# Performance work log

Measured on AMD Instinct MI355X. Metric: run time of the kernel, lower is better.

Reference implementation:

```python
import jax, jax.numpy as jnp
import numpy as np

B, T, C, H = 128, 256, 512, 2048
STEP_SIZE = 0.001
TOTAL = 1.0 / (T - 1)                       # uniform linspace(0,1,T) interval length
STEPS_HINT = max(1, int(TOTAL / STEP_SIZE))
N_SUB = max(1, int(max(STEPS_HINT, TOTAL / STEP_SIZE)))  # = 3 fixed RK4 substeps per interval
DT = TOTAL / N_SUB


def setup_inputs() -> dict:
    key = jax.random.key(0)
    ks = jax.random.split(key, 7)
    def lin_w(k, fi, fo):
        return (jax.random.uniform(k, (fi, fo), jnp.float32, -1.0, 1.0) / np.sqrt(fi)).astype(jnp.float32)
    def lin_b(k, fi, fo):
        return (jax.random.uniform(k, (fo,), jnp.float32, -1.0, 1.0) / np.sqrt(fi)).astype(jnp.float32)
    x = jax.random.normal(ks[0], (B, T, C), jnp.float32)
    return {
        "x": x,
        "W1": lin_w(ks[1], C, H), "b1": lin_b(ks[2], C, H),
        "W2": lin_w(ks[3], H, H), "b2": lin_b(ks[4], H, H),
        "W3": lin_w(ks[5], H, C), "b3": lin_b(ks[6], H, C),
    }


def _mlp(y, W1, b1, W2, b2, W3, b3):
    # f(y) = Linear(Tanh(Linear(Tanh(Linear(y)))))
    h = jnp.tanh(y @ W1 + b1)
    h = jnp.tanh(h @ W2 + b2)
    return h @ W3 + b3


def _rk4_step(y, dt, p):
    k1 = _mlp(y, *p)
    k2 = _mlp(y + 0.5 * dt * k1, *p)
    k3 = _mlp(y + 0.5 * dt * k2, *p)
    k4 = _mlp(y + dt * k3, *p)
    return y + (dt / 6.0) * (k1 + 2.0 * k2 + 2.0 * k3 + k4)


def reference(x, W1, b1, W2, b2, W3, b3):
    p = (W1, b1, W2, b2, W3, b3)
    def interval(y, _):
        for _ in range(N_SUB):  # static, small unroll (3)
            y = _rk4_step(y, DT, p)
        return y, y
    y0 = x[:, 0, :]                                   # [B, C]
    _, ys = jax.lax.scan(interval, y0, None, length=T - 1)  # ys: [T-1, B, C]
    return jnp.concatenate([x[:, :1, :], jnp.moveaxis(ys, 0, 1)], axis=1)  # [B, T, C]
```

## Files before the change

kernel.cpp:

```cpp
#include <hip/hip_runtime.h>
#include <hip/hip_bf16.h>
#include <cstdint>

#define B_ 128
#define T_ 256
#define C_ 512
#define H_ 2048
#define NWG 256
#define NTHR 256
#define NGROUP 8
#define GSIZE 32
#define M_ 16
#define FSTRIDE 16
#define RSU1 132
#define RSS1 528
#define DT_F 0.0013071895424836601f

typedef __bf16 bf16x8 __attribute__((ext_vector_type(8)));
typedef short s16x8 __attribute__((ext_vector_type(8)));
typedef float f32x4 __attribute__((ext_vector_type(4)));
typedef unsigned long long ull;

enum : size_t {
  OFF_FLAGS = 0,
  OFF_W1P = 32768,
  OFF_W2P = OFF_W1P + (size_t)C_ * H_ * 2,
  OFF_W3P = OFF_W2P + (size_t)H_ * H_ * 2,
  OFF_U   = OFF_W3P + (size_t)H_ * C_ * 2,
  OFF_H1  = OFF_U   + (size_t)NGROUP * M_ * C_ * 2,
  OFF_H2  = OFF_H1  + (size_t)NGROUP * M_ * H_ * 2,
  WS_END  = OFF_H2  + (size_t)NGROUP * M_ * H_ * 2
};

__device__ __forceinline__ bf16x8 ld_frag(const unsigned short* p) {
  s16x8 v = *reinterpret_cast<const s16x8*>(p);
  return __builtin_bit_cast(bf16x8, v);
}
__device__ __forceinline__ bf16x8 lds_frag(const unsigned short* p) {
  s16x8 v = *reinterpret_cast<const s16x8*>(p);
  return __builtin_bit_cast(bf16x8, v);
}
__device__ __forceinline__ void st_coh16(unsigned short* p, unsigned short v) {
  __hip_atomic_store(p, v, __ATOMIC_RELAXED, __HIP_MEMORY_SCOPE_AGENT);
}
__device__ __forceinline__ f32x4 mfma16(bf16x8 a, bf16x8 b, f32x4 c) {
  return __builtin_amdgcn_mfma_f32_16x16x32_bf16(a, b, c, 0, 0, 0);
}
__device__ __forceinline__ unsigned short tobf(float f) {
  return __builtin_bit_cast(unsigned short, (__bf16)f);
}
__device__ __forceinline__ float fast_tanh(float v) {
  float e = __expf(2.0f * v);
  return 1.0f - 2.0f / (e + 1.0f);
}

__global__ void init_flags_k(unsigned* f) {
  int i = blockIdx.x * 256 + threadIdx.x;
  if (i < NGROUP * GSIZE * FSTRIDE) f[i] = 0u;
}

__global__ void swizzle_w_k(const float* __restrict__ W, unsigned short* __restrict__ Wp,
                            int N, int kblog) {
  int idx = blockIdx.x * 256 + threadIdx.x;
  int j = idx & 7;
  int l = (idx >> 3) & 63;
  int rem = idx >> 9;
  int kb = rem & ((1 << kblog) - 1);
  int nt = rem >> kblog;
  int k = kb * 32 + ((l >> 4) << 3) + j;
  int n = (nt << 4) + (l & 15);
  Wp[idx] = tobf(W[(size_t)k * N + n]);
}

__device__ __forceinline__ void bar_arrive(unsigned* gf, int gn, unsigned gen) {
  asm volatile("s_waitcnt vmcnt(0)" ::: "memory");
  __syncthreads();
  if (threadIdx.x == 0)
    __hip_atomic_store(&gf[gn * FSTRIDE], gen, __ATOMIC_RELAXED, __HIP_MEMORY_SCOPE_AGENT);
}
__device__ __forceinline__ void bar_wait(unsigned* gf, unsigned gen) {
  if (threadIdx.x < GSIZE) {
    while (__hip_atomic_load(&gf[threadIdx.x * FSTRIDE], __ATOMIC_RELAXED,
                             __HIP_MEMORY_SCOPE_AGENT) < gen)
      __builtin_amdgcn_s_sleep(1);
  }
  __syncthreads();
}

__device__ __forceinline__ void issue_u(const ull* __restrict__ g, int tid, ull v[8]) {
  #pragma unroll
  for (int j = 0; j < 8; ++j)
    v[j] = __hip_atomic_load(g + j * NTHR + tid, __ATOMIC_RELAXED, __HIP_MEMORY_SCOPE_AGENT);
}
__device__ __forceinline__ void issue_c(const ull* __restrict__ g, int tid, ull v[8]) {
  #pragma unroll
  for (int j = 0; j < 8; ++j) {
    int i = j * NTHR + tid;
    v[j] = __hip_atomic_load(g + (size_t)(i >> 7) * 512 + (i & 127),
                             __ATOMIC_RELAXED, __HIP_MEMORY_SCOPE_AGENT);
  }
}
__device__ __forceinline__ void commit(ull* __restrict__ lds, int tid, const ull v[8]) {
  #pragma unroll
  for (int j = 0; j < 8; ++j) {
    int i = j * NTHR + tid;
    lds[(i >> 7) * RSU1 + (i & 127)] = v[j];
  }
}

#define L2CHUNK(c, buf) {                                                     \
  const unsigned short* al = (const unsigned short*)atile[buf] + llo * RSS1 + lhi * 8; \
  _Pragma("unroll")                                                           \
  for (int jj = 0; jj < 8; ++jj) {                                            \
    acc0 = mfma16(lds_frag(al + (2 * jj) * 32),     w2r[(c) * 16 + 2 * jj],     acc0); \
    acc1 = mfma16(lds_frag(al + (2 * jj + 1) * 32), w2r[(c) * 16 + 2 * jj + 1], acc1); \
  } }

#define L3CHUNK(c, buf) {                                                     \
  const unsigned short* al = (const unsigned short*)atile[buf] + llo * RSS1 + lhi * 8; \
  _Pragma("unroll")                                                           \
  for (int jj = 0; jj < 2; ++jj) {                                            \
    acc0 = mfma16(lds_frag(al + (wave * 4 + 2 * jj) * 32),     w3r[(c) * 4 + 2 * jj],     acc0); \
    acc1 = mfma16(lds_frag(al + (wave * 4 + 2 * jj + 1) * 32), w3r[(c) * 4 + 2 * jj + 1], acc1); \
  } }

__global__ __launch_bounds__(NTHR, 1) void ode_persist_k(
    const float* __restrict__ x, const float* __restrict__ b1,
    const float* __restrict__ b2, const float* __restrict__ b3,
    float* __restrict__ out, unsigned char* __restrict__ ws) {
  const int wg = blockIdx.x, tid = threadIdx.x;
  const int g = wg >> 5, gn = wg & 31;
  const int wave = tid >> 6, lane = tid & 63;
  const int lhi = lane >> 4, llo = lane & 15;

  unsigned* gflags = (unsigned*)(ws + OFF_FLAGS) + g * GSIZE * FSTRIDE;
  const unsigned short* W1p = (const unsigned short*)(ws + OFF_W1P);
  const unsigned short* W2p = (const unsigned short*)(ws + OFF_W2P);
  const unsigned short* W3p = (const unsigned short*)(ws + OFF_W3P);
  const ull* ubuf_u = (const ull*)(ws + OFF_U)  + (size_t)g * (M_ * C_ / 4);
  const ull* h1_u   = (const ull*)(ws + OFF_H1) + (size_t)g * (M_ * H_ / 4);
  const ull* h2_u   = (const ull*)(ws + OFF_H2) + (size_t)g * (M_ * H_ / 4);
  unsigned short* ubuf_s = (unsigned short*)(ws + OFF_U)  + (size_t)g * M_ * C_;
  unsigned short* h1_s   = (unsigned short*)(ws + OFF_H1) + (size_t)g * M_ * H_;
  unsigned short* h2_s   = (unsigned short*)(ws + OFF_H2) + (size_t)g * M_ * H_;

  __shared__ alignas(16) ull atile[2][M_ * RSU1];
  __shared__ float red[4][256];
  __shared__ float ytile[256], k1t[256], k2t[256], k3t[256];

  const int n16 = gn * 4 + wave;
  const unsigned short* bp1 = W1p + (size_t)n16 * 16 * 512 + lane * 8;
  const unsigned short* bp2 = W2p + (size_t)n16 * 64 * 512 + lane * 8;
  const unsigned short* bp3 = W3p + (size_t)gn  * 64 * 512 + lane * 8;

  bf16x8 w2r[64], w3r[16];
  #pragma unroll
  for (int kb = 0; kb < 64; ++kb) w2r[kb] = ld_frag(bp2 + kb * 512);
  #pragma unroll
  for (int q = 0; q < 16; ++q)
    w3r[q] = ld_frag(bp3 + ((q >> 2) * 16 + wave * 4 + (q & 3)) * 512);

  const float bb1 = b1[n16 * 16 + llo];
  const float bb2 = b2[n16 * 16 + llo];
  const float bb3 = b3[gn * 16 + llo];

  {
    int row = tid >> 4, c16 = tid & 15;
    int col = gn * 16 + c16;
    int b = g * M_ + row;
    float v = x[(size_t)b * (T_ * C_) + col];
    ytile[tid] = v;
    out[(size_t)b * (T_ * C_) + col] = v;
    st_coh16(&ubuf_s[row * C_ + col], tobf(v));
  }
  unsigned gen = 0;
  bar_arrive(gflags, gn, ++gen);
  bar_wait(gflags, gen);

  ull va[8], vb[8];
  #pragma unroll 1
  for (int t = 0; t < T_ - 1; ++t) {
    #pragma unroll 1
    for (int sub = 0; sub < 3; ++sub) {
      #pragma unroll 1
      for (int st = 0; st < 4; ++st) {
        {
          issue_u(ubuf_u, tid, va);
          bf16x8 w1f[16];
          #pragma unroll
          for (int kb = 0; kb < 16; ++kb) w1f[kb] = ld_frag(bp1 + kb * 512);
          commit(atile[0], tid, va);
          __syncthreads();
          f32x4 acc0 = {0.f, 0.f, 0.f, 0.f}, acc1 = {0.f, 0.f, 0.f, 0.f};
          const unsigned short* al = (const unsigned short*)atile[0] + llo * RSS1 + lhi * 8;
          #pragma unroll
          for (int jj = 0; jj < 8; ++jj) {
            acc0 = mfma16(lds_frag(al + (2 * jj) * 32),     w1f[2 * jj],     acc0);
            acc1 = mfma16(lds_frag(al + (2 * jj + 1) * 32), w1f[2 * jj + 1], acc1);
          }
          f32x4 a = acc0 + acc1;
          const int col = n16 * 16 + llo;
          #pragma unroll
          for (int r = 0; r < 4; ++r)
            st_coh16(&h1_s[(lhi * 4 + r) * H_ + col], tobf(fast_tanh(a[r] + bb1)));
        }
        bar_arrive(gflags, gn, ++gen);
        bar_wait(gflags, gen);

        {
          f32x4 acc0 = {0.f, 0.f, 0.f, 0.f}, acc1 = {0.f, 0.f, 0.f, 0.f};
          issue_c(h1_u,       tid, va);
          issue_c(h1_u + 128, tid, vb);
          commit(atile[0], tid, va);
          __syncthreads();
          issue_c(h1_u + 256, tid, va);
          L2CHUNK(0, 0);
          commit(atile[1], tid, vb);
          __syncthreads();
          issue_c(h1_u + 384, tid, vb);
          L2CHUNK(1, 1);
          commit(atile[0], tid, va);
          __syncthreads();
          L2CHUNK(2, 0);
          commit(atile[1], tid, vb);
          __syncthreads();
          L2CHUNK(3, 1);
          f32x4 a = acc0 + acc1;
          const int col = n16 * 16 + llo;
          #pragma unroll
          for (int r = 0; r < 4; ++r)
            st_coh16(&h2_s[(lhi * 4 + r) * H_ + col], tobf(fast_tanh(a[r] + bb2)));
        }
        bar_arrive(gflags, gn, ++gen);
        bar_wait(gflags, gen);

        {
          f32x4 acc0 = {0.f, 0.f, 0.f, 0.f}, acc1 = {0.f, 0.f, 0.f, 0.f};
          issue_c(h2_u,       tid, va);
          issue_c(h2_u + 128, tid, vb);
          commit(atile[0], tid, va);
          __syncthreads();
          issue_c(h2_u + 256, tid, va);
          L3CHUNK(0, 0);
          commit(atile[1], tid, vb);
          __syncthreads();
          issue_c(h2_u + 384, tid, vb);
          L3CHUNK(1, 1);
          commit(atile[0], tid, va);
          __syncthreads();
          L3CHUNK(2, 0);
          commit(atile[1], tid, vb);
          __syncthreads();
          L3CHUNK(3, 1);
          f32x4 a = acc0 + acc1;
          #pragma unroll
          for (int r = 0; r < 4; ++r) red[wave][(lhi * 4 + r) * 16 + llo] = a[r];
          __syncthreads();
          if (wave == 0) {
            const float dt = DT_F;
            #pragma unroll
            for (int r = 0; r < 4; ++r) {
              int row = lhi * 4 + r;
              int i = row * 16 + llo;
              float z = red[0][i] + red[1][i] + red[2][i] + red[3][i] + bb3;
              float yv = ytile[i];
              unsigned short* up = &ubuf_s[row * C_ + gn * 16 + llo];
              if (st == 0)      { k1t[i] = z; st_coh16(up, tobf(yv + 0.5f * dt * z)); }
              else if (st == 1) { k2t[i] = z; st_coh16(up, tobf(yv + 0.5f * dt * z)); }
              else if (st == 2) { k3t[i] = z; st_coh16(up, tobf(yv + dt * z)); }
              else {
                float yn = yv + (dt * (1.0f / 6.0f)) * (k1t[i] + 2.f * k2t[i] + 2.f * k3t[i] + z);
                ytile[i] = yn;
                st_coh16(up, tobf(yn));
                if (sub == 2)
                  out[(size_t)(g * M_ + row) * (T_ * C_) + (size_t)(t + 1) * C_ + gn * 16 + llo] = yn;
              }
            }
          }
        }
        bar_arrive(gflags, gn, ++gen);
        bar_wait(gflags, gen);
      }
    }
  }
}

extern "C" void kernel_launch(void* const* d_in, const int* in_sizes, int n_in,
                              void* d_out, int out_size, void* d_ws, size_t ws_size,
                              hipStream_t stream) {
  (void)in_sizes; (void)n_in; (void)out_size; (void)ws_size;
  const float* x  = (const float*)d_in[0];
  const float* W1 = (const float*)d_in[1];
  const float* b1 = (const float*)d_in[2];
  const float* W2 = (const float*)d_in[3];
  const float* b2 = (const float*)d_in[4];
  const float* W3 = (const float*)d_in[5];
  const float* b3 = (const float*)d_in[6];
  float* out = (float*)d_out;
  unsigned char* ws = (unsigned char*)d_ws;

  init_flags_k<<<16, 256, 0, stream>>>((unsigned*)(ws + OFF_FLAGS));
  swizzle_w_k<<<(C_ * H_) / 256, 256, 0, stream>>>(W1, (unsigned short*)(ws + OFF_W1P), H_, 4);
  swizzle_w_k<<<(H_ * H_) / 256, 256, 0, stream>>>(W2, (unsigned short*)(ws + OFF_W2P), H_, 6);
  swizzle_w_k<<<(H_ * C_) / 256, 256, 0, stream>>>(W3, (unsigned short*)(ws + OFF_W3P), C_, 6);

  ode_persist_k<<<NWG, NTHR, 0, stream>>>(x, b1, b2, b3, out, ws);
}
```

Baseline: 43.91 ms.

## Use XCD-local plain stores and sc0 loads for group exchange with coherence probe fallback

Workgroups are remapped so each group of 32 collaborators is interleaved by blockIdx (g = wg & 7), which presumably places a whole group on one XCD. The change then replaces agent-scope atomic stores and loads for activations and barrier flags with plain stores and sc0 loads that only need to stay coherent in the local L2. A startup probe checks that group members really see each other's plain writes. The barrier keeps a shadow agent-scope flag with a polling cap and a sticky fallback, which adds complexity and relies on the hardware placement holding.

```diff
diff --git a/kernel.cpp b/kernel.cpp
--- a/kernel.cpp
+++ b/kernel.cpp
@@ -15,6 +15,7 @@
 #define RSU1 132
 #define RSS1 528
 #define DT_F 0.0013071895424836601f
+#define POLL_CAP 8192
 
 typedef __bf16 bf16x8 __attribute__((ext_vector_type(8)));
 typedef short s16x8 __attribute__((ext_vector_type(8)));
@@ -23,7 +24,10 @@
 
 enum : size_t {
   OFF_FLAGS = 0,
-  OFF_W1P = 32768,
+  OFF_SHAD  = 16384,
+  OFF_PROBE = 32768,
+  OFF_OK    = 49152,
+  OFF_W1P   = 65536,
   OFF_W2P = OFF_W1P + (size_t)C_ * H_ * 2,
   OFF_W3P = OFF_W2P + (size_t)H_ * H_ * 2,
   OFF_U   = OFF_W3P + (size_t)H_ * C_ * 2,
@@ -40,8 +44,9 @@
   s16x8 v = *reinterpret_cast<const s16x8*>(p);
   return __builtin_bit_cast(bf16x8, v);
 }
-__device__ __forceinline__ void st_coh16(unsigned short* p, unsigned short v) {
-  __hip_atomic_store(p, v, __ATOMIC_RELAXED, __HIP_MEMORY_SCOPE_AGENT);
+__device__ __forceinline__ void st16(unsigned short* p, unsigned short v, bool fast) {
+  if (fast) *p = v;
+  else __hip_atomic_store(p, v, __ATOMIC_RELAXED, __HIP_MEMORY_SCOPE_AGENT);
 }
 __device__ __forceinline__ f32x4 mfma16(bf16x8 a, bf16x8 b, f32x4 c) {
   return __builtin_amdgcn_mfma_f32_16x16x32_bf16(a, b, c, 0, 0, 0);
@@ -53,10 +58,36 @@
   float e = __expf(2.0f * v);
   return 1.0f - 2.0f / (e + 1.0f);
 }
+__device__ __forceinline__ unsigned ld_sc0_u32(const unsigned* p) {
+  unsigned v;
+  asm volatile("global_load_dword %0, %1, off sc0\n\t"
+               "s_waitcnt vmcnt(0)"
+               : "=&v"(v) : "v"(p) : "memory");
+  return v;
+}
+__device__ __forceinline__ void issue8f(const ull* base, unsigned o0, unsigned stride, ull v[8]) {
+  unsigned a0 = o0,            a1 = o0 + stride,     a2 = o0 + 2 * stride, a3 = o0 + 3 * stride,
+           a4 = o0 + 4 * stride, a5 = o0 + 5 * stride, a6 = o0 + 6 * stride, a7 = o0 + 7 * stride;
+  asm volatile(
+      "global_load_dwordx2 %0, %8, %16 sc0\n\t"
+      "global_load_dwordx2 %1, %9, %16 sc0\n\t"
+      "global_load_dwordx2 %2, %10, %16 sc0\n\t"
+      "global_load_dwordx2 %3, %11, %16 sc0\n\t"
+      "global_load_dwordx2 %4, %12, %16 sc0\n\t"
+      "global_load_dwordx2 %5, %13, %16 sc0\n\t"
+      "global_load_dwordx2 %6, %14, %16 sc0\n\t"
+      "global_load_dwordx2 %7, %15, %16 sc0\n\t"
+      "s_waitcnt vmcnt(0)"
+      : "=&v"(v[0]), "=&v"(v[1]), "=&v"(v[2]), "=&v"(v[3]),
+        "=&v"(v[4]), "=&v"(v[5]), "=&v"(v[6]), "=&v"(v[7])
+      : "v"(a0), "v"(a1), "v"(a2), "v"(a3), "v"(a4), "v"(a5), "v"(a6), "v"(a7),
+        "s"(base)
+      : "memory");
+}
 
 __global__ void init_flags_k(unsigned* f) {
   int i = blockIdx.x * 256 + threadIdx.x;
-  if (i < NGROUP * GSIZE * FSTRIDE) f[i] = 0u;
+  if (i < 16384) f[i] = 0u;
 }
 
 __global__ void swizzle_w_k(const float* __restrict__ W, unsigned short* __restrict__ Wp,
@@ -72,32 +103,69 @@
   Wp[idx] = tobf(W[(size_t)k * N + n]);
 }
 
-__device__ __forceinline__ void bar_arrive(unsigned* gf, int gn, unsigned gen) {
+__device__ __forceinline__ void bar_arrive(unsigned* gf, unsigned* gs, int gn,
+                                           unsigned gen, bool fast) {
   asm volatile("s_waitcnt vmcnt(0)" ::: "memory");
   __syncthreads();
-  if (threadIdx.x == 0)
-    __hip_atomic_store(&gf[gn * FSTRIDE], gen, __ATOMIC_RELAXED, __HIP_MEMORY_SCOPE_AGENT);
-}
-__device__ __forceinline__ void bar_wait(unsigned* gf, unsigned gen) {
+  if (threadIdx.x == 0) {
+    if (fast) {
+      gf[gn * FSTRIDE] = gen;
+      __hip_atomic_store(&gs[gn * FSTRIDE], gen, __ATOMIC_RELAXED,
+                         __HIP_MEMORY_SCOPE_AGENT);
+    } else {
+      __hip_atomic_store(&gf[gn * FSTRIDE], gen, __ATOMIC_RELAXED,
+                         __HIP_MEMORY_SCOPE_AGENT);
+    }
+  }
+}
+__device__ __forceinline__ void bar_wait(unsigned* gf, unsigned* gs, unsigned gen,
+                                         bool fast, bool& sticky) {
   if (threadIdx.x < GSIZE) {
-    while (__hip_atomic_load(&gf[threadIdx.x * FSTRIDE], __ATOMIC_RELAXED,
-                             __HIP_MEMORY_SCOPE_AGENT) < gen)
-      __builtin_amdgcn_s_sleep(1);
+    const unsigned* fp = gf + threadIdx.x * FSTRIDE;
+    const unsigned* sp = gs + threadIdx.x * FSTRIDE;
+    if (fast && !sticky) {
+      int it = 0; bool done = false;
+      for (;;) {
+        if (ld_sc0_u32(fp) >= gen) { done = true; break; }
+        if (++it > POLL_CAP) break;
+        __builtin_amdgcn_s_sleep(1);
+      }
+      if (!done) {
+        while (__hip_atomic_load(sp, __ATOMIC_RELAXED, __HIP_MEMORY_SCOPE_AGENT) < gen)
+          __builtin_amdgcn_s_sleep(2);
+        if (ld_sc0_u32(fp) < gen) sticky = true;
+      }
+    } else if (fast) {
+      while (__hip_atomic_load(sp, __ATOMIC_RELAXED, __HIP_MEMORY_SCOPE_AGENT) < gen)
+        __builtin_amdgcn_s_sleep(1);
+    } else {
+      while (__hip_atomic_load(fp, __ATOMIC_RELAXED, __HIP_MEMORY_SCOPE_AGENT) < gen)
+        __builtin_amdgcn_s_sleep(1);
+    }
   }
   __syncthreads();
 }
 
-__device__ __forceinline__ void issue_u(const ull* __restrict__ g, int tid, ull v[8]) {
-  #pragma unroll
-  for (int j = 0; j < 8; ++j)
-    v[j] = __hip_atomic_load(g + j * NTHR + tid, __ATOMIC_RELAXED, __HIP_MEMORY_SCOPE_AGENT);
-}
-__device__ __forceinline__ void issue_c(const ull* __restrict__ g, int tid, ull v[8]) {
-  #pragma unroll
-  for (int j = 0; j < 8; ++j) {
-    int i = j * NTHR + tid;
-    v[j] = __hip_atomic_load(g + (size_t)(i >> 7) * 512 + (i & 127),
-                             __ATOMIC_RELAXED, __HIP_MEMORY_SCOPE_AGENT);
+__device__ __forceinline__ void issue_u(const ull* __restrict__ g, int tid, ull v[8], bool fast) {
+  if (fast) {
+    issue8f(g, (unsigned)(tid * 8), 2048u, v);
+  } else {
+    #pragma unroll
+    for (int j = 0; j < 8; ++j)
+      v[j] = __hip_atomic_load(g + j * NTHR + tid, __ATOMIC_RELAXED, __HIP_MEMORY_SCOPE_AGENT);
+  }
+}
+__device__ __forceinline__ void issue_c(const ull* __restrict__ g, int tid, ull v[8], bool fast) {
+  if (fast) {
+    unsigned o0 = (unsigned)((((tid >> 7) * 512) + (tid & 127)) * 8);
+    issue8f(g, o0, 8192u, v);
+  } else {
+    #pragma unroll
+    for (int j = 0; j < 8; ++j) {
+      int i = j * NTHR + tid;
+      v[j] = __hip_atomic_load(g + (size_t)(i >> 7) * 512 + (i & 127),
+                               __ATOMIC_RELAXED, __HIP_MEMORY_SCOPE_AGENT);
+    }
   }
 }
 __device__ __forceinline__ void commit(ull* __restrict__ lds, int tid, const ull v[8]) {
@@ -129,11 +197,14 @@
     const float* __restrict__ b2, const float* __restrict__ b3,
     float* __restrict__ out, unsigned char* __restrict__ ws) {
   const int wg = blockIdx.x, tid = threadIdx.x;
-  const int g = wg >> 5, gn = wg & 31;
+  const int g = wg & 7, gn = wg >> 3;
   const int wave = tid >> 6, lane = tid & 63;
   const int lhi = lane >> 4, llo = lane & 15;
 
   unsigned* gflags = (unsigned*)(ws + OFF_FLAGS) + g * GSIZE * FSTRIDE;
+  unsigned* gshad  = (unsigned*)(ws + OFF_SHAD)  + g * GSIZE * FSTRIDE;
+  unsigned* probe  = (unsigned*)(ws + OFF_PROBE) + g * GSIZE * FSTRIDE;
+  unsigned* okarr  = (unsigned*)(ws + OFF_OK)    + g * GSIZE * FSTRIDE;
   const unsigned short* W1p = (const unsigned short*)(ws + OFF_W1P);
   const unsigned short* W2p = (const unsigned short*)(ws + OFF_W2P);
   const unsigned short* W3p = (const unsigned short*)(ws + OFF_W3P);
@@ -147,6 +218,7 @@
   __shared__ alignas(16) ull atile[2][M_ * RSU1];
   __shared__ float red[4][256];
   __shared__ float ytile[256], k1t[256], k2t[256], k3t[256];
+  __shared__ int sh_ok;
 
   const int n16 = gn * 4 + wave;
   const unsigned short* bp1 = W1p + (size_t)n16 * 16 * 512 + lane * 8;
@@ -171,11 +243,41 @@
     float v = x[(size_t)b * (T_ * C_) + col];
     ytile[tid] = v;
     out[(size_t)b * (T_ * C_) + col] = v;
-    st_coh16(&ubuf_s[row * C_ + col], tobf(v));
-  }
+    __hip_atomic_store(&ubuf_s[row * C_ + col], tobf(v),
+                       __ATOMIC_RELAXED, __HIP_MEMORY_SCOPE_AGENT);
+  }
+  if (tid == 0) sh_ok = 1;
+  if (tid == 1) probe[gn * FSTRIDE] = 0xA5A50000u | (unsigned)(g << 8) | (unsigned)gn;
   unsigned gen = 0;
-  bar_arrive(gflags, gn, ++gen);
-  bar_wait(gflags, gen);
+  bool sticky = false;
+  bar_arrive(gflags, gshad, gn, ++gen, false);
+  bar_wait(gflags, gshad, gen, false, sticky);
+
+  {
+    bool myok = true;
+    if (tid < GSIZE) {
+      unsigned v = ld_sc0_u32(&probe[tid * FSTRIDE]);
+      myok = (v == (0xA5A50000u | (unsigned)(g << 8) | (unsigned)tid));
+    }
+    __syncthreads();
+    if (!myok) sh_ok = 0;
+    __syncthreads();
+    if (tid == 0)
+      __hip_atomic_store(&okarr[gn * FSTRIDE], sh_ok ? 2u : 1u,
+                         __ATOMIC_RELAXED, __HIP_MEMORY_SCOPE_AGENT);
+  }
+  bar_arrive(gflags, gshad, gn, ++gen, false);
+  bar_wait(gflags, gshad, gen, false, sticky);
+  {
+    bool myok = true;
+    if (tid < GSIZE)
+      myok = (__hip_atomic_load(&okarr[tid * FSTRIDE], __ATOMIC_RELAXED,
+                                __HIP_MEMORY_SCOPE_AGENT) == 2u);
+    __syncthreads();
+    if (!myok) sh_ok = 0;
+    __syncthreads();
+  }
+  const bool fast = sh_ok != 0;
 
   ull va[8], vb[8];
   #pragma unroll 1
@@ -185,7 +287,7 @@
       #pragma unroll 1
       for (int st = 0; st < 4; ++st) {
         {
-          issue_u(ubuf_u, tid, va);
+          issue_u(ubuf_u, tid, va, fast);
           bf16x8 w1f[16];
           #pragma unroll
           for (int kb = 0; kb < 16; ++kb) w1f[kb] = ld_frag(bp1 + kb * 512);
@@ -202,22 +304,22 @@
           const int col = n16 * 16 + llo;
           #pragma unroll
           for (int r = 0; r < 4; ++r)
-            st_coh16(&h1_s[(lhi * 4 + r) * H_ + col], tobf(fast_tanh(a[r] + bb1)));
+            st16(&h1_s[(lhi * 4 + r) * H_ + col], tobf(fast_tanh(a[r] + bb1)), fast);
         }
-        bar_arrive(gflags, gn, ++gen);
-        bar_wait(gflags, gen);
+        bar_arrive(gflags, gshad, gn, ++gen, fast);
+        bar_wait(gflags, gshad, gen, fast, sticky);
 
         {
           f32x4 acc0 = {0.f, 0.f, 0.f, 0.f}, acc1 = {0.f, 0.f, 0.f, 0.f};
-          issue_c(h1_u,       tid, va);
-          issue_c(h1_u + 128, tid, vb);
+          issue_c(h1_u,       tid, va, fast);
+          issue_c(h1_u + 128, tid, vb, fast);
           commit(atile[0], tid, va);
           __syncthreads();
-          issue_c(h1_u + 256, tid, va);
+          issue_c(h1_u + 256, tid, va, fast);
           L2CHUNK(0, 0);
           commit(atile[1], tid, vb);
           __syncthreads();
-          issue_c(h1_u + 384, tid, vb);
+          issue_c(h1_u + 384, tid, vb, fast);
           L2CHUNK(1, 1);
           commit(atile[0], tid, va);
           __syncthreads();
@@ -229,22 +331,22 @@
           const int col = n16 * 16 + llo;
           #pragma unroll
           for (int r = 0; r < 4; ++r)
-            st_coh16(&h2_s[(lhi * 4 + r) * H_ + col], tobf(fast_tanh(a[r] + bb2)));
+            st16(&h2_s[(lhi * 4 + r) * H_ + col], tobf(fast_tanh(a[r] + bb2)), fast);
         }
-        bar_arrive(gflags, gn, ++gen);
-        bar_wait(gflags, gen);
+        bar_arrive(gflags, gshad, gn, ++gen, fast);
+        bar_wait(gflags, gshad, gen, fast, sticky);
 
         {
           f32x4 acc0 = {0.f, 0.f, 0.f, 0.f}, acc1 = {0.f, 0.f, 0.f, 0.f};
-          issue_c(h2_u,       tid, va);
-          issue_c(h2_u + 128, tid, vb);
+          issue_c(h2_u,       tid, va, fast);
+          issue_c(h2_u + 128, tid, vb, fast);
           commit(atile[0], tid, va);
           __syncthreads();
-          issue_c(h2_u + 256, tid, va);
+          issue_c(h2_u + 256, tid, va, fast);
           L3CHUNK(0, 0);
           commit(atile[1], tid, vb);
           __syncthreads();
-          issue_c(h2_u + 384, tid, vb);
+          issue_c(h2_u + 384, tid, vb, fast);
           L3CHUNK(1, 1);
           commit(atile[0], tid, va);
           __syncthreads();
@@ -265,21 +367,21 @@
               float z = red[0][i] + red[1][i] + red[2][i] + red[3][i] + bb3;
               float yv = ytile[i];
               unsigned short* up = &ubuf_s[row * C_ + gn * 16 + llo];
-              if (st == 0)      { k1t[i] = z; st_coh16(up, tobf(yv + 0.5f * dt * z)); }
-              else if (st == 1) { k2t[i] = z; st_coh16(up, tobf(yv + 0.5f * dt * z)); }
-              else if (st == 2) { k3t[i] = z; st_coh16(up, tobf(yv + dt * z)); }
+              if (st == 0)      { k1t[i] = z; st16(up, tobf(yv + 0.5f * dt * z), fast); }
+              else if (st == 1) { k2t[i] = z; st16(up, tobf(yv + 0.5f * dt * z), fast); }
+              else if (st == 2) { k3t[i] = z; st16(up, tobf(yv + dt * z), fast); }
               else {
                 float yn = yv + (dt * (1.0f / 6.0f)) * (k1t[i] + 2.f * k2t[i] + 2.f * k3t[i] + z);
                 ytile[i] = yn;
-                st_coh16(up, tobf(yn));
+                st16(up, tobf(yn), fast);
                 if (sub == 2)
                   out[(size_t)(g * M_ + row) * (T_ * C_) + (size_t)(t + 1) * C_ + gn * 16 + llo] = yn;
               }
             }
           }
         }
-        bar_arrive(gflags, gn, ++gen);
-        bar_wait(gflags, gen);
+        bar_arrive(gflags, gshad, gn, ++gen, fast);
+        bar_wait(gflags, gshad, gen, fast, sticky);
       }
     }
   }
@@ -299,7 +401,7 @@
   float* out = (float*)d_out;
   unsigned char* ws = (unsigned char*)d_ws;
 
-  init_flags_k<<<16, 256, 0, stream>>>((unsigned*)(ws + OFF_FLAGS));
+  init_flags_k<<<64, 256, 0, stream>>>((unsigned*)(ws + OFF_FLAGS));
   swizzle_w_k<<<(C_ * H_) / 256, 256, 0, stream>>>(W1, (unsigned short*)(ws + OFF_W1P), H_, 4);
   swizzle_w_k<<<(H_ * H_) / 256, 256, 0, stream>>>(W2, (unsigned short*)(ws + OFF_W2P), H_, 6);
   swizzle_w_k<<<(H_ * C_) / 256, 256, 0, stream>>>(W3, (unsigned short*)(ws + OFF_W3P), C_, 6);
```

Result: slower. 49.62 ms (+13.0%).
